# Optimization experiments

Measured on AMD Instinct MI355X. Metric: run time of the kernel, lower is better.

## Reference

```python
import jax, jax.numpy as jnp
import numpy as np
from jax.scipy.special import xlogy

N = 8192
NUM_CLASSES = 100

def setup_inputs() -> dict:
    key = jax.random.key(0)
    k1, k2, k3 = jax.random.split(key, 3)
    pred1 = jax.random.normal(k1, (N, N), dtype=jnp.float32)
    pred2 = jax.random.normal(k2, (N, N), dtype=jnp.float32)
    labels = jax.random.randint(k3, (N,), 0, NUM_CLASSES, dtype=jnp.int64)
    return {"pred1": pred1, "pred2": pred2, "labels": labels}

def _kl_div_mean(log_input, target):
    # torch.nn.KLDivLoss(reduction='mean'): mean over ALL elements of
    # target * (log(target) - log_input), with 0*log(0) := 0 (xlogy).
    return jnp.mean(xlogy(target, target) - target * log_input)

def reference(pred1, pred2, labels):
    n = pred1.shape[0]
    # vectorized replacement of the python double loop: gt[i,k] = (labels[k]==labels[i])
    gt = (labels[None, :] == labels[:, None]).astype(pred1.dtype)
    probs3 = jax.nn.softmax(gt * 10.0, axis=1)  # [N,N] soft target rows
    logp1 = jax.nn.log_softmax(pred1, axis=1)
    logp2 = jax.nn.log_softmax(pred2, axis=1)
    loss1 = _kl_div_mean(logp1, probs3) * n
    loss2 = _kl_div_mean(logp2, probs3.T) * n
    return (loss1 + loss2) / 2.0
```

## Files before the change

kernel.cpp:

```cpp
#include <hip/hip_runtime.h>
#include <math.h>


constexpr int N_ = 8192;
constexpr int NCLS = 100;
constexpr int NCLSP = 128;
constexpr float E10F = 22026.465794806718f;
constexpr int GRID = 2048;
constexpr int ROWSPB = N_ / GRID;
constexpr int TILE = 4096;
constexpr int NSTEP = ROWSPB * 2;

__global__ void prep_kernel(const int* __restrict__ labels,
                            int* __restrict__ counts,
                            float* __restrict__ wcls,
                            float* __restrict__ Wout,
                            unsigned char* __restrict__ labu8) {
    __shared__ int cnt[NCLSP];
    int tid = threadIdx.x;
    if (tid < NCLSP) cnt[tid] = 0;
    __syncthreads();
    for (int i = tid; i < N_; i += blockDim.x) {
        int l = labels[i];
        labu8[i] = (unsigned char)l;
        atomicAdd(&cnt[l], 1);
    }
    __syncthreads();
    if (tid < NCLSP) {
        int c = cnt[tid];
        counts[tid] = c;
        float D = (float)c * E10F + (float)(N_ - c);
        wcls[tid] = 1.0f / D;
    }
    __syncthreads();
    if (tid == 0) {
        double W = 0.0;
        const double e10 = 22026.465794806718;
        for (int c = 0; c < NCLS; ++c) {
            double cc = (double)cnt[c];
            double D = cc * e10 + ((double)N_ - cc);
            W += cc / D;
        }
        Wout[0] = (float)W;
    }
}

__device__ __forceinline__ void stage16k(const float* __restrict__ g,
                                         float* lds, int lane, int wv) {
#pragma unroll
    for (int c = 0; c < 4; ++c) {
        const int chunk = wv + c * 4;
        __builtin_amdgcn_global_load_lds(
            (const __attribute__((address_space(1))) void*)(g + chunk * 256 + lane * 4),
            (__attribute__((address_space(3))) void*)(lds + chunk * 256),
            16, 0, 0);
    }
}

__launch_bounds__(256)
__global__ void row_kernel(const float* __restrict__ pred1,
                           const float* __restrict__ pred2,
                           const unsigned char* __restrict__ labu8,
                           const int* __restrict__ counts,
                           const float* __restrict__ wcls,
                           const float* __restrict__ Wptr,
                           float* __restrict__ contrib) {
    __shared__ float tA[2][TILE];
    __shared__ float tB[2][TILE];
    __shared__ unsigned char labs[N_];
    __shared__ float wshm[NCLSP];
    __shared__ int cnts[NCLSP];
    __shared__ float red[4][6];

    const int tid = threadIdx.x;
    const int lane = tid & 63, wv = tid >> 6;
    const int bid = blockIdx.x;

#pragma unroll
    for (int c = wv; c < 8; c += 4)
        __builtin_amdgcn_global_load_lds(
            (const __attribute__((address_space(1))) void*)(labu8 + c * 1024 + lane * 16),
            (__attribute__((address_space(3))) void*)(labs + c * 1024),
            16, 0, 0);
    if (tid < NCLSP) {
        wshm[tid] = wcls[tid];
        cnts[tid] = counts[tid];
    }
    stage16k(pred1 + (size_t)bid * N_, tA[0], lane, wv);
    stage16k(pred2 + (size_t)bid * N_, tB[0], lane, wv);
    const float W = Wptr[0];
    __syncthreads();

    float s1 = 0.f, s2 = 0.f, su1 = 0.f, su2 = 0.f, ms1 = 0.f, ms2 = 0.f;

    for (int s = 0; s < NSTEP; ++s) {
        const int p = s >> 1, t = s & 1, b = s & 1;
        const int r = bid + p * GRID;

        if (s + 1 < NSTEP) {
            const int p2 = (s + 1) >> 1, t2 = (s + 1) & 1;
            const size_t off = (size_t)(bid + p2 * GRID) * N_ + (size_t)t2 * TILE;
            stage16k(pred1 + off, tA[(s + 1) & 1], lane, wv);
            stage16k(pred2 + off, tB[(s + 1) & 1], lane, wv);
        }

        const int rowlab = (int)labs[r];
        const int base4 = (t * TILE) >> 2;
        const float4* A4 = (const float4*)tA[b];
        const float4* B4 = (const float4*)tB[b];
        const uchar4* L4 = (const uchar4*)labs;

#pragma unroll
        for (int k = 0; k < 4; ++k) {
            const int j = k * 256 + tid;
            float4 v = A4[j];
            float4 u = B4[j];
            uchar4 lb = L4[base4 + j];

            s1 += __expf(v.x) + __expf(v.y) + __expf(v.z) + __expf(v.w);
            s2 += __expf(u.x) + __expf(u.y) + __expf(u.z) + __expf(u.w);
            su1 += (v.x + v.y) + (v.z + v.w);

            float w0 = wshm[lb.x], w1 = wshm[lb.y], w2 = wshm[lb.z], w3 = wshm[lb.w];
            su2 = fmaf(u.x, w0, fmaf(u.y, w1, fmaf(u.z, w2, fmaf(u.w, w3, su2))));

            bool e0 = ((int)lb.x == rowlab), e1 = ((int)lb.y == rowlab);
            bool e2 = ((int)lb.z == rowlab), e3 = ((int)lb.w == rowlab);
            ms1 += (e0 ? v.x : 0.f) + (e1 ? v.y : 0.f) + (e2 ? v.z : 0.f) + (e3 ? v.w : 0.f);
            ms2 += (e0 ? u.x : 0.f) + (e1 ? u.y : 0.f) + (e2 ? u.z : 0.f) + (e3 ? u.w : 0.f);
        }

        if (t == 1) {
#pragma unroll
            for (int mask = 32; mask >= 1; mask >>= 1) {
                s1 += __shfl_xor(s1, mask, 64);
                s2 += __shfl_xor(s2, mask, 64);
                su1 += __shfl_xor(su1, mask, 64);
                su2 += __shfl_xor(su2, mask, 64);
                ms1 += __shfl_xor(ms1, mask, 64);
                ms2 += __shfl_xor(ms2, mask, 64);
            }
            if (lane == 0) {
                red[wv][0] = s1; red[wv][1] = s2; red[wv][2] = su1;
                red[wv][3] = su2; red[wv][4] = ms1; red[wv][5] = ms2;
            }
            __syncthreads();
            if (tid == 0) {
                float S1 = 0.f, S2 = 0.f, SU1 = 0.f, SU2 = 0.f, MS1 = 0.f, MS2 = 0.f;
#pragma unroll
                for (int q = 0; q < 4; ++q) {
                    S1 += red[q][0]; S2 += red[q][1]; SU1 += red[q][2];
                    SU2 += red[q][3]; MS1 += red[q][4]; MS2 += red[q][5];
                }
                float lse1 = logf(S1), lse2 = logf(S2);
                int cnt = cnts[rowlab];
                float w = wshm[rowlab];
                contrib[r] = w * (SU1 - (float)N_ * lse1) +
                             (E10F - 1.0f) * w * (MS1 - (float)cnt * lse1);
                contrib[N_ + r] = (SU2 - lse2 * W) +
                                  (E10F - 1.0f) * w * (MS2 - (float)cnt * lse2);
            }
            s1 = s2 = su1 = su2 = ms1 = ms2 = 0.f;
        }
        __syncthreads();
    }
}

__global__ void final_kernel(const int* __restrict__ counts,
                             const float* __restrict__ contrib,
                             float* __restrict__ out) {
    __shared__ double red[256];
    int tid = threadIdx.x;
    double acc = 0.0;
    for (int i = tid; i < 2 * N_; i += 256)
        acc += (double)contrib[i];
    red[tid] = acc;
    __syncthreads();
    for (int st = 128; st > 0; st >>= 1) {
        if (tid < st) red[tid] += red[tid + st];
        __syncthreads();
    }
    if (tid == 0) {
        const double e10 = 22026.465794806718;
        double H = 0.0;
        for (int c = 0; c < NCLS; ++c) {
            double cc = (double)counts[c];
            double D = cc * e10 + ((double)N_ - cc);
            double logD = log(D);
            H += cc * (cc * (e10 / D) * (10.0 - logD) +
                       ((double)N_ - cc) * (1.0 / D) * (-logD));
        }
        out[0] = (float)((2.0 * H - red[0]) / (2.0 * (double)N_));
    }
}

extern "C" void kernel_launch(void* const* d_in, const int* in_sizes, int n_in,
                              void* d_out, int out_size, void* d_ws, size_t ws_size,
                              hipStream_t stream) {
    const float* pred1 = (const float*)d_in[0];
    const float* pred2 = (const float*)d_in[1];
    const int* labels = (const int*)d_in[2];
    float* out = (float*)d_out;

    float* wsf = (float*)d_ws;
    int* wsi = (int*)d_ws;
    int* counts = wsi;
    float* wcls = wsf + 128;
    float* Wptr = wsf + 256;
    unsigned char* labu8 = (unsigned char*)(wsf + 384);
    float* contrib = wsf + 2560;

    prep_kernel<<<1, 1024, 0, stream>>>(labels, counts, wcls, Wptr, labu8);
    row_kernel<<<GRID, 256, 0, stream>>>(pred1, pred2, labu8, counts, wcls,
                                         Wptr, contrib);
    final_kernel<<<1, 256, 0, stream>>>(counts, contrib, out);
}
```

Measured before the change: 161.2 us.

## Deepen row kernel pipeline to four buffers with contiguous row blocks

Row kernel now runs 512 blocks, each handling 16 contiguous rows in 2048-float tiles. A 4-deep LDS ring keeps three tiles in flight, using explicit vmcnt waits and raw s_barrier in place of full __syncthreads each step. Per-row results are buffered in LDS and written once at the end. The aim is better overlap of HBM loads with compute and lower sync overhead. In exchange there are fewer blocks, so less occupancy-based latency hiding, and correctness now depends on hand-counted waitcnt values.

```diff
diff --git a/kernel.cpp b/kernel.cpp
--- a/kernel.cpp
+++ b/kernel.cpp
@@ -6,10 +6,12 @@
 constexpr int NCLS = 100;
 constexpr int NCLSP = 128;
 constexpr float E10F = 22026.465794806718f;
-constexpr int GRID = 2048;
+constexpr int GRID = 512;
 constexpr int ROWSPB = N_ / GRID;
-constexpr int TILE = 4096;
-constexpr int NSTEP = ROWSPB * 2;
+constexpr int TILE = 2048;
+constexpr int TPR = N_ / TILE;
+constexpr int NSTEP = ROWSPB * TPR;
+constexpr int NBUF = 4;
 
 __global__ void prep_kernel(const int* __restrict__ labels,
                             int* __restrict__ counts,
@@ -45,11 +47,11 @@
     }
 }
 
-__device__ __forceinline__ void stage16k(const float* __restrict__ g,
-                                         float* lds, int lane, int wv) {
-#pragma unroll
-    for (int c = 0; c < 4; ++c) {
-        const int chunk = wv + c * 4;
+__device__ __forceinline__ void stage_tile(const float* __restrict__ g,
+                                           float* lds, int lane, int wv) {
+#pragma unroll
+    for (int c = 0; c < 2; ++c) {
+        const int chunk = wv * 2 + c;
         __builtin_amdgcn_global_load_lds(
             (const __attribute__((address_space(1))) void*)(g + chunk * 256 + lane * 4),
             (__attribute__((address_space(3))) void*)(lds + chunk * 256),
@@ -65,57 +67,76 @@
                            const float* __restrict__ wcls,
                            const float* __restrict__ Wptr,
                            float* __restrict__ contrib) {
-    __shared__ float tA[2][TILE];
-    __shared__ float tB[2][TILE];
+    __shared__ float tA[NBUF][TILE];
+    __shared__ float tB[NBUF][TILE];
     __shared__ unsigned char labs[N_];
     __shared__ float wshm[NCLSP];
     __shared__ int cnts[NCLSP];
     __shared__ float red[4][6];
+    __shared__ float cres[ROWSPB][2];
 
     const int tid = threadIdx.x;
     const int lane = tid & 63, wv = tid >> 6;
     const int bid = blockIdx.x;
-
-#pragma unroll
-    for (int c = wv; c < 8; c += 4)
-        __builtin_amdgcn_global_load_lds(
-            (const __attribute__((address_space(1))) void*)(labu8 + c * 1024 + lane * 16),
-            (__attribute__((address_space(3))) void*)(labs + c * 1024),
-            16, 0, 0);
+    const int rowbase = bid * ROWSPB;
+
     if (tid < NCLSP) {
         wshm[tid] = wcls[tid];
         cnts[tid] = counts[tid];
     }
-    stage16k(pred1 + (size_t)bid * N_, tA[0], lane, wv);
-    stage16k(pred2 + (size_t)bid * N_, tB[0], lane, wv);
     const float W = Wptr[0];
     __syncthreads();
 
+#pragma unroll
+    for (int c = 0; c < 2; ++c) {
+        const int chunk = wv * 2 + c;
+        __builtin_amdgcn_global_load_lds(
+            (const __attribute__((address_space(1))) void*)(labu8 + chunk * 1024 + lane * 16),
+            (__attribute__((address_space(3))) void*)(labs + chunk * 1024),
+            16, 0, 0);
+    }
+#pragma unroll
+    for (int s = 0; s < 3; ++s) {
+        const size_t off = (size_t)(rowbase + (s >> 2)) * N_ + (size_t)(s & 3) * TILE;
+        stage_tile(pred1 + off, tA[s & 3], lane, wv);
+        stage_tile(pred2 + off, tB[s & 3], lane, wv);
+    }
+
     float s1 = 0.f, s2 = 0.f, su1 = 0.f, su2 = 0.f, ms1 = 0.f, ms2 = 0.f;
 
     for (int s = 0; s < NSTEP; ++s) {
-        const int p = s >> 1, t = s & 1, b = s & 1;
-        const int r = bid + p * GRID;
-
-        if (s + 1 < NSTEP) {
-            const int p2 = (s + 1) >> 1, t2 = (s + 1) & 1;
-            const size_t off = (size_t)(bid + p2 * GRID) * N_ + (size_t)t2 * TILE;
-            stage16k(pred1 + off, tA[(s + 1) & 1], lane, wv);
-            stage16k(pred2 + off, tB[(s + 1) & 1], lane, wv);
-        }
-
+        if (s < NSTEP - 2)
+            asm volatile("s_waitcnt vmcnt(8)" ::: "memory");
+        else if (s == NSTEP - 2)
+            asm volatile("s_waitcnt vmcnt(4)" ::: "memory");
+        else
+            asm volatile("s_waitcnt vmcnt(0)" ::: "memory");
+        __builtin_amdgcn_sched_barrier(0);
+        __builtin_amdgcn_s_barrier();
+        __builtin_amdgcn_sched_barrier(0);
+
+        if (s + 3 < NSTEP) {
+            const int s3 = s + 3;
+            const size_t off = (size_t)(rowbase + (s3 >> 2)) * N_ + (size_t)(s3 & 3) * TILE;
+            stage_tile(pred1 + off, tA[s3 & 3], lane, wv);
+            stage_tile(pred2 + off, tB[s3 & 3], lane, wv);
+        }
+        __builtin_amdgcn_sched_barrier(0);
+
+        const int p = s >> 2, t = s & 3, b = s & 3;
+        const int r = rowbase + p;
         const int rowlab = (int)labs[r];
-        const int base4 = (t * TILE) >> 2;
         const float4* A4 = (const float4*)tA[b];
         const float4* B4 = (const float4*)tB[b];
         const uchar4* L4 = (const uchar4*)labs;
-
-#pragma unroll
-        for (int k = 0; k < 4; ++k) {
+        const int lbase = t * (TILE / 4);
+
+#pragma unroll
+        for (int k = 0; k < 2; ++k) {
             const int j = k * 256 + tid;
             float4 v = A4[j];
             float4 u = B4[j];
-            uchar4 lb = L4[base4 + j];
+            uchar4 lb = L4[lbase + j];
 
             s1 += __expf(v.x) + __expf(v.y) + __expf(v.z) + __expf(v.w);
             s2 += __expf(u.x) + __expf(u.y) + __expf(u.z) + __expf(u.w);
@@ -130,7 +151,7 @@
             ms2 += (e0 ? u.x : 0.f) + (e1 ? u.y : 0.f) + (e2 ? u.z : 0.f) + (e3 ? u.w : 0.f);
         }
 
-        if (t == 1) {
+        if ((s & 3) == 3) {
 #pragma unroll
             for (int mask = 32; mask >= 1; mask >>= 1) {
                 s1 += __shfl_xor(s1, mask, 64);
@@ -144,7 +165,9 @@
                 red[wv][0] = s1; red[wv][1] = s2; red[wv][2] = su1;
                 red[wv][3] = su2; red[wv][4] = ms1; red[wv][5] = ms2;
             }
-            __syncthreads();
+            asm volatile("s_waitcnt lgkmcnt(0)" ::: "memory");
+            __builtin_amdgcn_s_barrier();
+            __builtin_amdgcn_sched_barrier(0);
             if (tid == 0) {
                 float S1 = 0.f, S2 = 0.f, SU1 = 0.f, SU2 = 0.f, MS1 = 0.f, MS2 = 0.f;
 #pragma unroll
@@ -155,14 +178,20 @@
                 float lse1 = logf(S1), lse2 = logf(S2);
                 int cnt = cnts[rowlab];
                 float w = wshm[rowlab];
-                contrib[r] = w * (SU1 - (float)N_ * lse1) +
+                cres[p][0] = w * (SU1 - (float)N_ * lse1) +
                              (E10F - 1.0f) * w * (MS1 - (float)cnt * lse1);
-                contrib[N_ + r] = (SU2 - lse2 * W) +
-                                  (E10F - 1.0f) * w * (MS2 - (float)cnt * lse2);
+                cres[p][1] = (SU2 - lse2 * W) +
+                             (E10F - 1.0f) * w * (MS2 - (float)cnt * lse2);
             }
             s1 = s2 = su1 = su2 = ms1 = ms2 = 0.f;
         }
-        __syncthreads();
+    }
+
+    __syncthreads();
+    if (tid < ROWSPB) {
+        const int r = rowbase + tid;
+        contrib[r] = cres[tid][0];
+        contrib[N_ + r] = cres[tid][1];
     }
 }
 
```

Measured after the change: 169.6 us. +5.2%, slower.

## Replace LDS staging with register double-buffered nontemporal loads and deferred reductions

Applied to the files above, without the earlier changes.

Drops the global_load_lds double-buffered shared-memory staging of pred tiles. Each thread now prefetches the next half-row into registers with nontemporal loads while computing on the current one. Blocks now own contiguous rows instead of grid-strided rows. Per-row partial sums are kept in register arrays and reduced once at the end, removing the per-step __syncthreads barriers. The cost is more registers, which may lower occupancy, and load latency is hidden only one segment ahead.

```diff
diff --git a/kernel.cpp b/kernel.cpp
--- a/kernel.cpp
+++ b/kernel.cpp
@@ -1,6 +1,8 @@
 #include <hip/hip_runtime.h>
 #include <math.h>
 
+
+typedef float f4 __attribute__((ext_vector_type(4)));
 
 constexpr int N_ = 8192;
 constexpr int NCLS = 100;
@@ -8,8 +10,7 @@
 constexpr float E10F = 22026.465794806718f;
 constexpr int GRID = 2048;
 constexpr int ROWSPB = N_ / GRID;
-constexpr int TILE = 4096;
-constexpr int NSTEP = ROWSPB * 2;
+constexpr int SEG = ROWSPB * 2;
 
 __global__ void prep_kernel(const int* __restrict__ labels,
                             int* __restrict__ counts,
@@ -45,18 +46,6 @@
     }
 }
 
-__device__ __forceinline__ void stage16k(const float* __restrict__ g,
-                                         float* lds, int lane, int wv) {
-#pragma unroll
-    for (int c = 0; c < 4; ++c) {
-        const int chunk = wv + c * 4;
-        __builtin_amdgcn_global_load_lds(
-            (const __attribute__((address_space(1))) void*)(g + chunk * 256 + lane * 4),
-            (__attribute__((address_space(3))) void*)(lds + chunk * 256),
-            16, 0, 0);
-    }
-}
-
 __launch_bounds__(256)
 __global__ void row_kernel(const float* __restrict__ pred1,
                            const float* __restrict__ pred2,
@@ -65,104 +54,125 @@
                            const float* __restrict__ wcls,
                            const float* __restrict__ Wptr,
                            float* __restrict__ contrib) {
-    __shared__ float tA[2][TILE];
-    __shared__ float tB[2][TILE];
     __shared__ unsigned char labs[N_];
     __shared__ float wshm[NCLSP];
     __shared__ int cnts[NCLSP];
-    __shared__ float red[4][6];
+    __shared__ float red[4][ROWSPB][6];
 
     const int tid = threadIdx.x;
     const int lane = tid & 63, wv = tid >> 6;
-    const int bid = blockIdx.x;
-
-#pragma unroll
-    for (int c = wv; c < 8; c += 4)
+    const int rowbase = blockIdx.x * ROWSPB;
+
+#pragma unroll
+    for (int c = 0; c < 2; ++c) {
+        const int chunk = wv * 2 + c;
         __builtin_amdgcn_global_load_lds(
-            (const __attribute__((address_space(1))) void*)(labu8 + c * 1024 + lane * 16),
-            (__attribute__((address_space(3))) void*)(labs + c * 1024),
+            (const __attribute__((address_space(1))) void*)(labu8 + chunk * 1024 + lane * 16),
+            (__attribute__((address_space(3))) void*)(labs + chunk * 1024),
             16, 0, 0);
+    }
     if (tid < NCLSP) {
         wshm[tid] = wcls[tid];
         cnts[tid] = counts[tid];
     }
-    stage16k(pred1 + (size_t)bid * N_, tA[0], lane, wv);
-    stage16k(pred2 + (size_t)bid * N_, tB[0], lane, wv);
     const float W = Wptr[0];
     __syncthreads();
 
-    float s1 = 0.f, s2 = 0.f, su1 = 0.f, su2 = 0.f, ms1 = 0.f, ms2 = 0.f;
-
-    for (int s = 0; s < NSTEP; ++s) {
-        const int p = s >> 1, t = s & 1, b = s & 1;
-        const int r = bid + p * GRID;
-
-        if (s + 1 < NSTEP) {
-            const int p2 = (s + 1) >> 1, t2 = (s + 1) & 1;
-            const size_t off = (size_t)(bid + p2 * GRID) * N_ + (size_t)t2 * TILE;
-            stage16k(pred1 + off, tA[(s + 1) & 1], lane, wv);
-            stage16k(pred2 + off, tB[(s + 1) & 1], lane, wv);
-        }
-
-        const int rowlab = (int)labs[r];
-        const int base4 = (t * TILE) >> 2;
-        const float4* A4 = (const float4*)tA[b];
-        const float4* B4 = (const float4*)tB[b];
-        const uchar4* L4 = (const uchar4*)labs;
-
+    float s1[ROWSPB], s2[ROWSPB], su1[ROWSPB], su2[ROWSPB], ms1[ROWSPB], ms2[ROWSPB];
+#pragma unroll
+    for (int rr = 0; rr < ROWSPB; ++rr)
+        s1[rr] = s2[rr] = su1[rr] = su2[rr] = ms1[rr] = ms2[rr] = 0.f;
+
+    const uchar4* L4 = (const uchar4*)labs;
+
+    f4 ca[4], cb[4], na[4], nb[4];
+
+    {
+        const f4* A4 = (const f4*)(pred1 + (size_t)rowbase * N_);
+        const f4* B4 = (const f4*)(pred2 + (size_t)rowbase * N_);
 #pragma unroll
         for (int k = 0; k < 4; ++k) {
-            const int j = k * 256 + tid;
-            float4 v = A4[j];
-            float4 u = B4[j];
-            uchar4 lb = L4[base4 + j];
-
-            s1 += __expf(v.x) + __expf(v.y) + __expf(v.z) + __expf(v.w);
-            s2 += __expf(u.x) + __expf(u.y) + __expf(u.z) + __expf(u.w);
-            su1 += (v.x + v.y) + (v.z + v.w);
+            ca[k] = __builtin_nontemporal_load(A4 + k * 256 + tid);
+            cb[k] = __builtin_nontemporal_load(B4 + k * 256 + tid);
+        }
+    }
+
+#pragma unroll
+    for (int s = 0; s < SEG; ++s) {
+        const int rr = s >> 1, half = s & 1;
+
+        if (s + 1 < SEG) {
+            const int rn = (s + 1) >> 1, hn = (s + 1) & 1;
+            const f4* A4 = (const f4*)(pred1 + (size_t)(rowbase + rn) * N_);
+            const f4* B4 = (const f4*)(pred2 + (size_t)(rowbase + rn) * N_);
+#pragma unroll
+            for (int k = 0; k < 4; ++k) {
+                na[k] = __builtin_nontemporal_load(A4 + hn * 1024 + k * 256 + tid);
+                nb[k] = __builtin_nontemporal_load(B4 + hn * 1024 + k * 256 + tid);
+            }
+        }
+        __builtin_amdgcn_sched_barrier(0);
+
+        const int rowlab = (int)labs[rowbase + rr];
+#pragma unroll
+        for (int k = 0; k < 4; ++k) {
+            const int j = half * 1024 + k * 256 + tid;
+            uchar4 lb = L4[j];
+            f4 v = ca[k], u = cb[k];
+
+            s1[rr] += __expf(v.x) + __expf(v.y) + __expf(v.z) + __expf(v.w);
+            s2[rr] += __expf(u.x) + __expf(u.y) + __expf(u.z) + __expf(u.w);
+            su1[rr] += (v.x + v.y) + (v.z + v.w);
 
             float w0 = wshm[lb.x], w1 = wshm[lb.y], w2 = wshm[lb.z], w3 = wshm[lb.w];
-            su2 = fmaf(u.x, w0, fmaf(u.y, w1, fmaf(u.z, w2, fmaf(u.w, w3, su2))));
+            su2[rr] = fmaf(u.x, w0, fmaf(u.y, w1, fmaf(u.z, w2, fmaf(u.w, w3, su2[rr]))));
 
             bool e0 = ((int)lb.x == rowlab), e1 = ((int)lb.y == rowlab);
             bool e2 = ((int)lb.z == rowlab), e3 = ((int)lb.w == rowlab);
-            ms1 += (e0 ? v.x : 0.f) + (e1 ? v.y : 0.f) + (e2 ? v.z : 0.f) + (e3 ? v.w : 0.f);
-            ms2 += (e0 ? u.x : 0.f) + (e1 ? u.y : 0.f) + (e2 ? u.z : 0.f) + (e3 ? u.w : 0.f);
-        }
-
-        if (t == 1) {
-#pragma unroll
-            for (int mask = 32; mask >= 1; mask >>= 1) {
-                s1 += __shfl_xor(s1, mask, 64);
-                s2 += __shfl_xor(s2, mask, 64);
-                su1 += __shfl_xor(su1, mask, 64);
-                su2 += __shfl_xor(su2, mask, 64);
-                ms1 += __shfl_xor(ms1, mask, 64);
-                ms2 += __shfl_xor(ms2, mask, 64);
-            }
-            if (lane == 0) {
-                red[wv][0] = s1; red[wv][1] = s2; red[wv][2] = su1;
-                red[wv][3] = su2; red[wv][4] = ms1; red[wv][5] = ms2;
-            }
-            __syncthreads();
-            if (tid == 0) {
-                float S1 = 0.f, S2 = 0.f, SU1 = 0.f, SU2 = 0.f, MS1 = 0.f, MS2 = 0.f;
-#pragma unroll
-                for (int q = 0; q < 4; ++q) {
-                    S1 += red[q][0]; S2 += red[q][1]; SU1 += red[q][2];
-                    SU2 += red[q][3]; MS1 += red[q][4]; MS2 += red[q][5];
-                }
-                float lse1 = logf(S1), lse2 = logf(S2);
-                int cnt = cnts[rowlab];
-                float w = wshm[rowlab];
-                contrib[r] = w * (SU1 - (float)N_ * lse1) +
-                             (E10F - 1.0f) * w * (MS1 - (float)cnt * lse1);
-                contrib[N_ + r] = (SU2 - lse2 * W) +
-                                  (E10F - 1.0f) * w * (MS2 - (float)cnt * lse2);
-            }
-            s1 = s2 = su1 = su2 = ms1 = ms2 = 0.f;
-        }
-        __syncthreads();
+            ms1[rr] += (e0 ? v.x : 0.f) + (e1 ? v.y : 0.f) + (e2 ? v.z : 0.f) + (e3 ? v.w : 0.f);
+            ms2[rr] += (e0 ? u.x : 0.f) + (e1 ? u.y : 0.f) + (e2 ? u.z : 0.f) + (e3 ? u.w : 0.f);
+        }
+
+        if (s + 1 < SEG) {
+#pragma unroll
+            for (int k = 0; k < 4; ++k) { ca[k] = na[k]; cb[k] = nb[k]; }
+        }
+    }
+
+#pragma unroll
+    for (int rr = 0; rr < ROWSPB; ++rr) {
+#pragma unroll
+        for (int mask = 32; mask >= 1; mask >>= 1) {
+            s1[rr] += __shfl_xor(s1[rr], mask, 64);
+            s2[rr] += __shfl_xor(s2[rr], mask, 64);
+            su1[rr] += __shfl_xor(su1[rr], mask, 64);
+            su2[rr] += __shfl_xor(su2[rr], mask, 64);
+            ms1[rr] += __shfl_xor(ms1[rr], mask, 64);
+            ms2[rr] += __shfl_xor(ms2[rr], mask, 64);
+        }
+        if (lane == 0) {
+            red[wv][rr][0] = s1[rr]; red[wv][rr][1] = s2[rr];
+            red[wv][rr][2] = su1[rr]; red[wv][rr][3] = su2[rr];
+            red[wv][rr][4] = ms1[rr]; red[wv][rr][5] = ms2[rr];
+        }
+    }
+    __syncthreads();
+    if (tid < ROWSPB) {
+        const int r = rowbase + tid;
+        float S1 = 0.f, S2 = 0.f, SU1 = 0.f, SU2 = 0.f, MS1 = 0.f, MS2 = 0.f;
+#pragma unroll
+        for (int q = 0; q < 4; ++q) {
+            S1 += red[q][tid][0]; S2 += red[q][tid][1]; SU1 += red[q][tid][2];
+            SU2 += red[q][tid][3]; MS1 += red[q][tid][4]; MS2 += red[q][tid][5];
+        }
+        float lse1 = logf(S1), lse2 = logf(S2);
+        const int rl = (int)labs[r];
+        int cnt = cnts[rl];
+        float w = wshm[rl];
+        contrib[r] = w * (SU1 - (float)N_ * lse1) +
+                     (E10F - 1.0f) * w * (MS1 - (float)cnt * lse1);
+        contrib[N_ + r] = (SU2 - lse2 * W) +
+                          (E10F - 1.0f) * w * (MS2 - (float)cnt * lse2);
     }
 }
 
```

Result: faster. 155.7 us (-3.4%).
